# Performance work log

Measured on AMD Instinct MI355X. Metric: run time of the kernel, lower is better.

Reference implementation:

```python
import jax, jax.numpy as jnp
import numpy as np

ALPHA, BETA, LAMB, GAMMA = 1.0, 1.0, 1e-4, 1.0
K_NN, TAU = 50, 0.1
EPS = 1e-8


def _sqdist(A, B):
    # ||a - b||^2, clamped at 0 like the torch code
    d2 = (A * A).sum(1)[:, None] + (B * B).sum(1)[None, :] - 2.0 * (A @ B.T)
    return jnp.maximum(d2, 0.0)


def _mmd(s, t):
    comb = jnp.concatenate([s, t], axis=0)
    sigma_sq = jax.lax.stop_gradient(jnp.median(_sqdist(comb, comb))) / 2.0
    sigma_sq = jnp.where(sigma_sq < 1e-6, jnp.float32(1.0), sigma_sq)
    g = 1.0 / (sigma_sq + EPS)
    kxx = jnp.exp(-g * _sqdist(s, s)).mean()
    kyy = jnp.exp(-g * _sqdist(t, t)).mean()
    kxy = jnp.exp(-g * _sqdist(s, t)).mean()
    return jnp.maximum(kxx + kyy - 2.0 * kxy, 0.0)


def setup_inputs() -> dict:
    key = jax.random.key(0)
    ks = jax.random.split(key, 8)
    B, d, N, Nq, K = 256, 128, 200000, 10000, K_NN
    q_batch = jax.random.normal(ks[0], (B, d), jnp.float32)
    X = jax.random.normal(ks[1], (N, d), jnp.float32)
    W = jax.random.normal(ks[2], (d, d), jnp.float32) * (1.0 / np.sqrt(d))
    b = jnp.zeros((d,), jnp.float32)
    pre_weights = jax.random.uniform(ks[3], (Nq, K), jnp.float32)
    pre_weights = pre_weights / pre_weights.sum(1, keepdims=True)
    pre_indices = jax.random.randint(ks[4], (Nq, K), 0, N)
    q_indices = jax.random.randint(ks[5], (B,), 0, Nq)
    idx = jax.random.randint(ks[6], (B,), 0, N)
    return {"q_batch": q_batch, "X": X, "W": W, "b": b,
            "pre_weights": pre_weights, "pre_indices": pre_indices,
            "q_indices": q_indices, "idx": idx}


def reference(q_batch, X, W, b, pre_weights, pre_indices, q_indices, idx):
    Tq = q_batch @ W.T + b                                   # model(q_batch), Linear(d, d)
    # ---- MMD between mapped queries and a random database batch ----
    loss_dist = _mmd(Tq, X[idx])
    # ---- exact KNN (faiss IndexFlatL2 equivalent) on detached embeddings ----
    d2_all = _sqdist(jax.lax.stop_gradient(Tq), X)           # [B, N]
    _, post_idx = jax.lax.top_k(-d2_all, K_NN)               # [B, K] nearest neighbors
    Xn = X[post_idx]                                         # [B, K, d]
    l2 = ((Tq[:, None, :] - Xn) ** 2).sum(-1)                # [B, K] (grad flows here)
    post_w = jax.nn.softmax(-l2 / TAU, axis=1)
    # ---- union-KL, vectorized over batch (exact torch.unique semantics) ----
    pre_i = pre_indices[q_indices]                           # [B, K]
    pre_w = pre_weights[q_indices]                           # [B, K]
    cat = jnp.concatenate([pre_i, post_idx], axis=1)         # [B, 2K]
    # multiplicity of each id within the concatenated list -> collapse duplicates
    mult = (cat[:, :, None] == cat[:, None, :]).sum(-1).astype(jnp.float32)  # [B, 2K]
    p_raw = jnp.einsum('bmk,bk->bm',
                       (cat[:, :, None] == pre_i[:, None, :]).astype(jnp.float32), pre_w)
    q_raw = jnp.einsum('bmk,bk->bm',
                       (cat[:, :, None] == post_idx[:, None, :]).astype(jnp.float32), post_w)
    p_c = jnp.maximum(p_raw, EPS)
    q_c = jnp.maximum(q_raw, EPS)
    p = p_c / (p_c / mult).sum(1, keepdims=True)             # normalize over union
    q = q_c / (q_c / mult).sum(1, keepdims=True)
    kl = ((p * (jnp.log(p) - jnp.log(q))) / mult).sum(1)     # KL(p || q) per sample
    loss_knn = kl.mean()
    # ---- L2 regularization of model params & anchor loss ----
    loss_reg = 0.5 * ((W ** 2).sum() + (b ** 2).sum())
    loss_anchor = ((Tq - q_batch) ** 2).sum(1).mean()
    total = ALPHA * loss_dist + BETA * loss_knn + LAMB * loss_reg + GAMMA * loss_anchor
    return jnp.stack([total, loss_dist, loss_knn, loss_anchor])
```

## Files before the change

kernel.cpp:

```cpp
#include <hip/hip_runtime.h>
#include <cstdint>

#define D 128
#define NPTS 200000
#define KNN 50
#define CAP 8192
#define NS 8192
#define SLACK 2.0f
#define EB 2048

#define OFF_ACC    0
#define OFF_SEL    256
#define OFF_CNT    1024
#define OFF_HIST0  17408
#define OFF_HIST12 148480
#define MEMSET_BYTES 214016
#define OFF_COMB   214016
#define OFF_D2     476160
#define OFF_XN     1524736
#define OFF_SAMP   2324736
#define OFF_EBUF   2324736
#define OFF_THR    10713344
#define OFF_CANDI  10714368
#define OFF_KSG    19102976
#define OFF_BCNT   19102976
#define OFF_TQSW   27491584
#define OFF_XBF    27557120

typedef __attribute__((ext_vector_type(8))) short bf16x8;
typedef __attribute__((ext_vector_type(4))) float f32x4;
typedef const __attribute__((address_space(1))) void* gas_p;
typedef __attribute__((address_space(3))) void* las_p;

__device__ __forceinline__ unsigned fkey(float f) {
    unsigned u = __float_as_uint(f);
    return u ^ ((unsigned)((int)u >> 31) | 0x80000000u);
}

__device__ __forceinline__ void stage8k(const unsigned short* __restrict__ g,
                                        unsigned short* l, int w, int lane)
{
    #pragma unroll
    for (int j = 0; j < 2; j++) {
        const unsigned short* gp = g + j * 2048 + w * 512 + lane * 8;
        unsigned short* lp = l + j * 2048 + w * 512;
        __builtin_amdgcn_global_load_lds((gas_p)gp, (las_p)lp, 16, 0, 0);
    }
}

__global__ void k_phase1(const float* __restrict__ q, const float* __restrict__ X,
                         const float* __restrict__ W, const float* __restrict__ bb,
                         const int* __restrict__ idx, float* __restrict__ comb,
                         unsigned short* __restrict__ tqsw, unsigned short* __restrict__ xbf,
                         float* __restrict__ xn, float* __restrict__ acc)
{
    const int blk = blockIdx.x, t = threadIdx.x;
    if (blk < 12500) {
        __shared__ float xr[16];
        const int lr = t & 15;
        if (t < 16) xr[t] = 0.f;
        __syncthreads();
        const float4* src = (const float4*)(X + ((long)(blk * 16 + lr)) * D + (t >> 4) * 8);
        float4 v0 = src[0], v1 = src[1];
        uint4 pk;
        pk.x = (__float_as_uint(v0.x) >> 16) | (__float_as_uint(v0.y) & 0xFFFF0000u);
        pk.y = (__float_as_uint(v0.z) >> 16) | (__float_as_uint(v0.w) & 0xFFFF0000u);
        pk.z = (__float_as_uint(v1.x) >> 16) | (__float_as_uint(v1.y) & 0xFFFF0000u);
        pk.w = (__float_as_uint(v1.z) >> 16) | (__float_as_uint(v1.w) & 0xFFFF0000u);
        *(uint4*)(xbf + (long)blk * 2048 + t * 8) = pk;
        float ssq = v0.x*v0.x + v0.y*v0.y + v0.z*v0.z + v0.w*v0.w
                  + v1.x*v1.x + v1.y*v1.y + v1.z*v1.z + v1.w*v1.w;
        atomicAdd(&xr[lr], ssq);
        __syncthreads();
        if (t < 16) xn[blk * 16 + t] = xr[t];
    } else if (blk < 12628) {
        __shared__ float rowv[2][D];
        __shared__ float red[2][D];
        const int half = t >> 7, tt = t & 127;
        const int row = (blk - 12500) * 2 + half;
        rowv[half][tt] = q[row * D + tt];
        __syncthreads();
        float s = 0.f;
        const float* wr = W + tt * D;
        #pragma unroll 4
        for (int k = 0; k < D; k++) s = fmaf(rowv[half][k], wr[k], s);
        s += bb[tt];
        comb[row * D + tt] = s;
        unsigned ub = __float_as_uint(s);
        unsigned short hv = (unsigned short)((ub + 0x7fffu + ((ub >> 16) & 1u)) >> 16);
        int ksb = tt >> 5, quad = (tt & 31) >> 3, jj = tt & 7;
        int lane = quad * 16 + (row & 15);
        tqsw[(row >> 4) * 2048 + ksb * 512 + lane * 8 + jj] = hv;
        float dd = s - rowv[half][tt];
        red[half][tt] = dd * dd;
        __syncthreads();
        for (int off = 64; off > 0; off >>= 1) { if (tt < off) red[half][tt] += red[half][tt + off]; __syncthreads(); }
        if (tt == 0) atomicAdd(&acc[0], red[half][0]);
    } else if (blk < 12756) {
        const int half = t >> 7, tt = t & 127;
        const int i = (blk - 12628) * 2 + half;
        comb[(256 + i) * D + tt] = X[(long)idx[i] * D + tt];
    } else {
        __shared__ float wred[4];
        const int base = (blk - 12756) * 4096;
        float s = 0.f;
        #pragma unroll 4
        for (int k = 0; k < 16; k++) { float v = W[base + k * 256 + t]; s = fmaf(v, v, s); }
        if (blk == 12756 && t < D) { float v = bb[t]; s = fmaf(v, v, s); }
        #pragma unroll
        for (int off = 32; off > 0; off >>= 1) s += __shfl_down(s, off);
        if ((t & 63) == 0) wred[t >> 6] = s;
        __syncthreads();
        if (t == 0) atomicAdd(&acc[7], wred[0] + wred[1] + wred[2] + wred[3]);
    }
}

__global__ void k_d2m(const float* __restrict__ comb, float* __restrict__ D2w,
                      unsigned* __restrict__ hist0, const unsigned short* __restrict__ tqsw,
                      const unsigned short* __restrict__ xbf, const float* __restrict__ xn,
                      float* __restrict__ samp)
{
    __shared__ __align__(16) char smraw[51456];
    const int b = blockIdx.x, t = threadIdx.x;
    if (b < 1024) {
        float (*cj)[D + 1] = (float(*)[D + 1])smraw;
        float (*ci)[D]     = (float(*)[D])(smraw + 33024);
        unsigned* h        = (unsigned*)(smraw + 35072);
        const int ib = b >> 3, jb = b & 7;
        const int w = t >> 6, l = t & 63;
        for (int m = t; m < 4096; m += 256) h[m] = 0;
        const int irow = ib * 4 + w;
        ci[w][l] = comb[irow * D + l];
        ci[w][l + 64] = comb[irow * D + l + 64];
        const float4* src = (const float4*)(comb + (jb * 64) * D);
        #pragma unroll
        for (int m = 0; m < 8; m++) {
            int u = m * 256 + t;
            int r = u >> 5, c = u & 31;
            float4 v = src[u];
            cj[r][c * 4 + 0] = v.x; cj[r][c * 4 + 1] = v.y; cj[r][c * 4 + 2] = v.z; cj[r][c * 4 + 3] = v.w;
        }
        __syncthreads();
        float s = 0.f;
        #pragma unroll 4
        for (int k = 0; k < D; k++) { float d = ci[w][k] - cj[l][k]; s = fmaf(d, d, s); }
        D2w[irow * 512 + jb * 64 + l] = s;
        atomicAdd(&h[__float_as_uint(s) >> 20], 1u);
        __syncthreads();
        const int sh = (ib + jb) & 7;
        for (int m = t; m < 4096; m += 256) { unsigned v = h[m]; if (v) atomicAdd(&hist0[m * 8 + sh], v); }
    } else {
        unsigned short* sb = (unsigned short*)smraw;
        const int w = t >> 6, lane = t & 63;
        const int lr = lane & 15, quad = lane >> 4;
        const int ck = b - 1024;
        stage8k(xbf + (long)ck * 4096, sb, w, lane);
        bf16x8 a[4][4];
        #pragma unroll
        for (int i = 0; i < 4; i++)
            #pragma unroll
            for (int ks = 0; ks < 4; ks++)
                a[i][ks] = *(const bf16x8*)(tqsw + (w * 4 + i) * 2048 + ks * 512 + lane * 8);
        __syncthreads();
        #pragma unroll
        for (int tt = 0; tt < 2; tt++) {
            const int r = (ck * 2 + tt) * 16 + lr;
            float xnv = xn[r];
            bf16x8 bfr[4];
            #pragma unroll
            for (int ks = 0; ks < 4; ks++)
                bfr[ks] = *(const bf16x8*)(sb + tt * 2048 + ks * 512 + lane * 8);
            f32x4 acc4[4];
            #pragma unroll
            for (int i = 0; i < 4; i++) acc4[i] = (f32x4){0.f, 0.f, 0.f, 0.f};
            #pragma unroll
            for (int ks = 0; ks < 4; ks++)
                #pragma unroll
                for (int i = 0; i < 4; i++)
                    acc4[i] = __builtin_amdgcn_mfma_f32_16x16x32_bf16(a[i][ks], bfr[ks], acc4[i], 0, 0, 0);
            #pragma unroll
            for (int i = 0; i < 4; i++)
                #pragma unroll
                for (int reg = 0; reg < 4; reg++) {
                    int qq = w * 64 + i * 16 + quad * 4 + reg;
                    samp[qq * NS + r] = xnv - 2.f * acc4[i][reg];
                }
        }
    }
}

__global__ void k_h1thr(const float* __restrict__ D2w, unsigned* __restrict__ hist12,
                        const unsigned* __restrict__ hist0, unsigned* __restrict__ sel,
                        const float* __restrict__ samp, float* __restrict__ thr)
{
    __shared__ unsigned buf[8192];
    __shared__ unsigned bins[4096];
    __shared__ unsigned part[256];
    __shared__ unsigned selll[4];
    __shared__ unsigned wred[4];
    const int t = threadIdx.x;
    if (blockIdx.x < 256) {
        unsigned s = 0;
        #pragma unroll
        for (int m = 0; m < 16; m++) {
            int bin = t * 16 + m;
            unsigned bs = 0;
            #pragma unroll
            for (int sh = 0; sh < 8; sh++) bs += hist0[bin * 8 + sh];
            bins[bin] = bs;
            s += bs;
        }
        part[t] = s;
        for (int m = t; m < 8192; m += 256) buf[m] = 0;
        __syncthreads();
        if (t == 0) {
            for (int tg = 0; tg < 2; tg++) {
                unsigned r = tg ? 131072u : 131071u;
                int c = 0;
                while (part[c] <= r) { r -= part[c]; c++; }
                int b = c * 16;
                while (bins[b] <= r) { r -= bins[b]; b++; }
                selll[2 * tg] = (unsigned)b; selll[2 * tg + 1] = r;
            }
            if (blockIdx.x == 0) {
                sel[0] = selll[0]; sel[1] = selll[1]; sel[2] = selll[2]; sel[3] = selll[3];
            }
        }
        __syncthreads();
        unsigned p0 = selll[0], p1 = selll[2];
        const int e0 = blockIdx.x * 1024;
        for (int m = 0; m < 4; m++) {
            unsigned key = __float_as_uint(D2w[e0 + m * 256 + t]);
            if ((key >> 20) == p0) atomicAdd(&buf[(key >> 8) & 0xFFFu], 1u);
            if ((key >> 20) == p1) atomicAdd(&buf[4096 + ((key >> 8) & 0xFFFu)], 1u);
        }
        __syncthreads();
        for (int m = t; m < 8192; m += 256) { unsigned v = buf[m]; if (v) atomicAdd(&hist12[m], v); }
    } else {
        const int q = blockIdx.x - 256;
        for (int m = t; m < NS; m += 256) buf[m] = fkey(samp[q * NS + m]);
        __syncthreads();
        unsigned v = 0;
        for (int bit = 31; bit >= 0; bit--) {
            unsigned trial = v | (1u << bit);
            unsigned c = 0;
            for (int m = t; m < NS; m += 256) c += (buf[m] < trial) ? 1u : 0u;
            #pragma unroll
            for (int off = 32; off > 0; off >>= 1) c += __shfl_down(c, off);
            if ((t & 63) == 0) wred[t >> 6] = c;
            __syncthreads();
            unsigned total = wred[0] + wred[1] + wred[2] + wred[3];
            __syncthreads();
            if (total <= (unsigned)(KNN - 1)) v = trial;
        }
        if (t == 0) {
            unsigned orig = (v & 0x80000000u) ? (v ^ 0x80000000u) : ~v;
            thr[q] = __uint_as_float(orig) + SLACK;
        }
    }
}

__global__ void k_hist2s(const float* __restrict__ D2w, unsigned* __restrict__ hist12,
                         unsigned* __restrict__ sel)
{
    __shared__ unsigned h[8192];
    __shared__ unsigned part[256];
    __shared__ unsigned pfx[2];
    __shared__ unsigned rr[2];
    const int t = threadIdx.x;
    for (int tg = 0; tg < 2; tg++) {
        const unsigned* hh = hist12 + tg * 4096;
        unsigned s = 0;
        for (int m = 0; m < 16; m++) s += hh[t * 16 + m];
        part[t] = s;
        __syncthreads();
        if (t == 0) {
            unsigned r = sel[1 + 2 * tg];
            int c = 0;
            while (part[c] <= r) { r -= part[c]; c++; }
            int b = c * 16;
            while (hh[b] <= r) { r -= hh[b]; b++; }
            pfx[tg] = (sel[2 * tg] << 12) | (unsigned)b;
            rr[tg] = r;
        }
        __syncthreads();
    }
    if (blockIdx.x == 0 && t == 0) {
        sel[4] = pfx[0]; sel[5] = rr[0]; sel[6] = pfx[1]; sel[7] = rr[1];
    }
    for (int m = t; m < 8192; m += 256) h[m] = 0;
    __syncthreads();
    unsigned p0 = pfx[0], p1 = pfx[1];
    const int e0 = blockIdx.x * 1024;
    for (int m = 0; m < 4; m++) {
        unsigned key = __float_as_uint(D2w[e0 + m * 256 + t]);
        if ((key >> 8) == p0) atomicAdd(&h[key & 0xFFu], 1u);
        if ((key >> 8) == p1) atomicAdd(&h[4096 + (key & 0xFFu)], 1u);
    }
    __syncthreads();
    unsigned* gp = hist12 + 8192;
    for (int m = t; m < 8192; m += 256) { unsigned v = h[m]; if (v) atomicAdd(&gp[m], v); }
}

__global__ __launch_bounds__(256) void k_mf1(const unsigned short* __restrict__ tqsw,
    const unsigned short* __restrict__ xbf, const float* __restrict__ xn,
    const float* __restrict__ thr, unsigned* __restrict__ ebuf, unsigned* __restrict__ bcnt,
    const float* __restrict__ D2w, const unsigned* __restrict__ hist12,
    const unsigned* __restrict__ sel, float* __restrict__ acc)
{
    if (blockIdx.x >= 1024) {
        __shared__ unsigned h2[512];
        __shared__ float gsh;
        __shared__ float part[12];
        const int t = threadIdx.x, w = t >> 6;
        h2[t] = hist12[8192 + t];
        h2[256 + t] = hist12[8192 + 4096 + t];
        __syncthreads();
        if (t == 0) {
            unsigned key[2];
            for (int tg = 0; tg < 2; tg++) {
                unsigned r = sel[5 + 2 * tg];
                const unsigned* hh = h2 + tg * 256;
                int b = 0;
                while (hh[b] <= r) { r -= hh[b]; b++; }
                key[tg] = (sel[4 + 2 * tg] << 8) | (unsigned)b;
            }
            float med = 0.5f * (__uint_as_float(key[0]) + __uint_as_float(key[1]));
            float ssq = 0.5f * med;
            if (ssq < 1e-6f) ssq = 1.0f;
            gsh = 1.0f / (ssq + 1e-8f);
        }
        __syncthreads();
        const float g = gsh;
        float s[3] = {0.f, 0.f, 0.f};
        const int e0 = (blockIdx.x - 1024) * 1024;
        #pragma unroll
        for (int m = 0; m < 4; m++) {
            int e = e0 + m * 256 + t;
            int i = e >> 9, j = e & 511;
            float v = expf(-g * D2w[e]);
            int qd = (i < 256) ? ((j < 256) ? 0 : 2) : ((j < 256) ? 2 : 1);
            s[qd] += v;
        }
        #pragma unroll
        for (int c = 0; c < 3; c++) {
            float x = s[c];
            #pragma unroll
            for (int off = 32; off > 0; off >>= 1) x += __shfl_down(x, off);
            if ((t & 63) == 0) part[w * 3 + c] = x;
        }
        __syncthreads();
        if (t == 0)
            for (int c = 0; c < 3; c++)
                atomicAdd(&acc[2 + c], part[c] + part[3 + c] + part[6 + c] + part[9 + c]);
        return;
    }
    __shared__ unsigned short sb[2][4096];
    __shared__ unsigned lbuf[1024];
    __shared__ unsigned lcnt;
    __shared__ unsigned gbase;
    const int t = threadIdx.x;
    const int w = t >> 6, lane = t & 63;
    const int lr = lane & 15, quad = lane >> 4;
    unsigned* eb = ebuf + (unsigned)blockIdx.x * EB;
    bf16x8 a[4][4];
    #pragma unroll
    for (int i = 0; i < 4; i++)
        #pragma unroll
        for (int ks = 0; ks < 4; ks++)
            a[i][ks] = *(const bf16x8*)(tqsw + (w * 4 + i) * 2048 + ks * 512 + lane * 8);
    float th_r[4][4];
    #pragma unroll
    for (int i = 0; i < 4; i++)
        #pragma unroll
        for (int reg = 0; reg < 4; reg++)
            th_r[i][reg] = thr[w * 64 + i * 16 + quad * 4 + reg];
    int ck = blockIdx.x;
    int cur = 0;
    if (t == 0) { lcnt = 0; gbase = 0; }
    stage8k(xbf + (long)ck * 4096, sb[0], w, lane);
    __syncthreads();
    while (true) {
        const int ckn = ck + 1024;
        const bool has = ckn < 6250;
        if (has) stage8k(xbf + (long)ckn * 4096, sb[cur ^ 1], w, lane);
        #pragma unroll
        for (int tt = 0; tt < 2; tt++) {
            const int r = (ck * 2 + tt) * 16 + lr;
            float xnv = xn[r];
            bf16x8 b[4];
            #pragma unroll
            for (int ks = 0; ks < 4; ks++)
                b[ks] = *(const bf16x8*)(sb[cur] + tt * 2048 + ks * 512 + lane * 8);
            f32x4 acc4[4];
            #pragma unroll
            for (int i = 0; i < 4; i++) acc4[i] = (f32x4){0.f, 0.f, 0.f, 0.f};
            #pragma unroll
            for (int ks = 0; ks < 4; ks++)
                #pragma unroll
                for (int i = 0; i < 4; i++)
                    acc4[i] = __builtin_amdgcn_mfma_f32_16x16x32_bf16(a[i][ks], b[ks], acc4[i], 0, 0, 0);
            #pragma unroll
            for (int i = 0; i < 4; i++)
                #pragma unroll
                for (int reg = 0; reg < 4; reg++) {
                    float s = xnv - 2.f * acc4[i][reg];
                    if (s <= th_r[i][reg]) {
                        unsigned qq = (unsigned)(w * 64 + i * 16 + quad * 4 + reg);
                        unsigned p = atomicAdd(&lcnt, 1u);
                        if (p < 1024u) lbuf[p] = (qq << 18) | (unsigned)r;
                        else {
                            unsigned d = gbase + p;
                            if (d < EB) eb[d] = (qq << 18) | (unsigned)r;
                        }
                    }
                }
        }
        __syncthreads();
        unsigned n = lcnt;
        if (!has || n >= 512u) {
            unsigned nf = (n < 1024u) ? n : 1024u;
            unsigned gb = gbase;
            for (unsigned m = t; m < nf; m += 256) {
                unsigned d = gb + m;
                if (d < EB) eb[d] = lbuf[m];
            }
            __syncthreads();
            if (t == 0) { gbase = gb + n; lcnt = 0; }
            __syncthreads();
        }
        if (!has) break;
        ck = ckn; cur ^= 1;
    }
    if (t == 0) bcnt[blockIdx.x] = (gbase < EB) ? gbase : EB;
}

__global__ __launch_bounds__(256) void k_scat(const unsigned* __restrict__ ebuf,
    const unsigned* __restrict__ bcnt, int* __restrict__ cand_i, unsigned* __restrict__ cnt)
{
    __shared__ unsigned hist[256];
    __shared__ unsigned startp[256];
    const int t = threadIdx.x;
    const int b0 = blockIdx.x * 8;
    hist[t] = 0;
    __syncthreads();
    for (int b = b0; b < b0 + 8; b++) {
        unsigned n = bcnt[b];
        const unsigned* e = ebuf + (unsigned)b * EB;
        for (unsigned m = t; m < n; m += 256)
            atomicAdd(&hist[e[m] >> 18], 1u);
    }
    __syncthreads();
    unsigned c = hist[t];
    if (c) {
        unsigned base = atomicAdd(&cnt[t * 16], c);
        startp[t] = ((unsigned)t << 13) + base;
    }
    __syncthreads();
    for (int b = b0; b < b0 + 8; b++) {
        unsigned n = bcnt[b];
        const unsigned* e = ebuf + (unsigned)b * EB;
        for (unsigned m = t; m < n; m += 256) {
            unsigned ent = e[m];
            unsigned qq = ent >> 18;
            unsigned pos = atomicAdd(&startp[qq], 1u);
            if (pos < ((qq + 1u) << 13)) cand_i[pos] = (int)(ent & 0x3FFFFu);
        }
    }
}

__global__ void k_rescore(const float* __restrict__ comb, const float* __restrict__ X,
                          const float* __restrict__ xn, const int* __restrict__ cand_i,
                          const unsigned* __restrict__ cnt, unsigned* __restrict__ ksg)
{
    __shared__ float qrow[D];
    const int q = blockIdx.x, sp = blockIdx.y, t = threadIdx.x;
    if (t < D) qrow[t] = comb[q * D + t];
    __syncthreads();
    unsigned nn = cnt[q * 16];
    const int n = (nn < (unsigned)CAP) ? (int)nn : CAP;
    const int g = t >> 3, j = t & 7;
    for (int m = sp * 32 + g; m < n; m += 512) {
        int r = cand_i[q * CAP + m];
        const float4* xr = (const float4*)(X + (long)r * D);
        float s = 0.f;
        #pragma unroll
        for (int p = 0; p < 4; p++) {
            float4 xv = xr[j * 4 + p];
            float4 qv = *(const float4*)&qrow[(j * 4 + p) * 4];
            s = fmaf(xv.x, qv.x, fmaf(xv.y, qv.y, fmaf(xv.z, qv.z, fmaf(xv.w, qv.w, s))));
        }
        s += __shfl_down(s, 4); s += __shfl_down(s, 2); s += __shfl_down(s, 1);
        if (j == 0) ksg[q * CAP + m] = fkey(xn[r] - 2.f * s);
    }
}

__global__ void k_post2(const float* __restrict__ comb, const float* __restrict__ X,
                        const int* __restrict__ cand_i, const unsigned* __restrict__ cnt,
                        const unsigned* __restrict__ ksg, const int* __restrict__ pri,
                        const float* __restrict__ prw, const int* __restrict__ qix,
                        float* __restrict__ acc)
{
    __shared__ unsigned ks[CAP];
    __shared__ float qrow[D];
    __shared__ unsigned wred[4];
    __shared__ unsigned wpos, eqn;
    __shared__ int eq[64];
    __shared__ int pidx[KNN];
    __shared__ float l2s[KNN];
    __shared__ float pw[KNN];
    __shared__ int ci[100];
    __shared__ float pwv[50], qwv[50];
    __shared__ float pterm[100], qterm[100], kterm[100];
    __shared__ float Sp, Sq;
    const int q = blockIdx.x, t = threadIdx.x;
    if (t < D) qrow[t] = comb[q * D + t];
    if (t == 0) { wpos = 0; eqn = 0; }
    unsigned nn = cnt[q * 16];
    const int n = (nn < (unsigned)CAP) ? (int)nn : CAP;
    for (int m = t; m < n; m += 256) ks[m] = ksg[q * CAP + m];
    __syncthreads();
    int kk = KNN - 1; if (kk > n - 1) kk = n - 1;
    unsigned v = 0;
    for (int bit = 31; bit >= 0; bit--) {
        unsigned trial = v | (1u << bit);
        unsigned c = 0;
        for (int m = t; m < n; m += 256) c += (ks[m] < trial) ? 1u : 0u;
        #pragma unroll
        for (int off = 32; off > 0; off >>= 1) c += __shfl_down(c, off);
        if ((t & 63) == 0) wred[t >> 6] = c;
        __syncthreads();
        unsigned total = wred[0] + wred[1] + wred[2] + wred[3];
        __syncthreads();
        if (total <= (unsigned)kk) v = trial;
    }
    for (int m = t; m < n; m += 256) {
        if (ks[m] < v) {
            unsigned p = atomicAdd(&wpos, 1u);
            pidx[p] = cand_i[q * CAP + m];
        } else if (ks[m] == v) {
            unsigned p = atomicAdd(&eqn, 1u);
            if (p < 64) eq[p] = cand_i[q * CAP + m];
        }
    }
    __syncthreads();
    if (t == 0) {
        int c1 = (int)wpos, need = KNN - c1;
        int ne = (eqn < 64u) ? (int)eqn : 64;
        for (int a = 0; a < ne; a++)
            for (int b2 = a + 1; b2 < ne; b2++)
                if (eq[b2] < eq[a]) { int tmp = eq[a]; eq[a] = eq[b2]; eq[b2] = tmp; }
        for (int a = 0; a < need && a < ne; a++) pidx[c1 + a] = eq[a];
    }
    __syncthreads();
    const int g = t >> 3, j = t & 7;
    for (int nb = g; nb < KNN; nb += 32) {
        long r = pidx[nb];
        const float4* xr = (const float4*)(X + r * D);
        float s = 0.f;
        #pragma unroll
        for (int p = 0; p < 4; p++) {
            float4 xv = xr[j * 4 + p];
            float4 qv = *(const float4*)&qrow[(j * 4 + p) * 4];
            float d0 = qv.x - xv.x, d1 = qv.y - xv.y, d2 = qv.z - xv.z, d3 = qv.w - xv.w;
            s += d0 * d0 + d1 * d1 + d2 * d2 + d3 * d3;
        }
        s += __shfl_down(s, 4); s += __shfl_down(s, 2); s += __shfl_down(s, 1);
        if (j == 0) l2s[nb] = s;
    }
    int qi = qix[q];
    if (t >= 128 && t < 178) { int k = t - 128; ci[k] = pri[qi * 50 + k]; pwv[k] = prw[qi * 50 + k]; }
    __syncthreads();
    if (t < 64) {
        float logit = (t < KNN) ? (-l2s[t] * 10.0f) : -3.4e38f;
        float m = logit;
        #pragma unroll
        for (int off = 32; off > 0; off >>= 1) m = fmaxf(m, __shfl_down(m, off));
        m = __shfl(m, 0);
        float e = (t < KNN) ? expf(logit - m) : 0.f;
        float ss = e;
        #pragma unroll
        for (int off = 32; off > 0; off >>= 1) ss += __shfl_down(ss, off);
        ss = __shfl(ss, 0);
        if (t < KNN) pw[t] = e / ss;
    }
    __syncthreads();
    if (t < 50) { ci[50 + t] = pidx[t]; qwv[t] = pw[t]; }
    __syncthreads();
    float pc = 0.f, qc = 0.f, mult = 0.f;
    if (t < 100) {
        int c = ci[t];
        float pr = 0.f, qr = 0.f;
        for (int k = 0; k < 50; k++) {
            bool m1 = (c == ci[k]); bool m2 = (c == ci[50 + k]);
            mult += (m1 ? 1.f : 0.f) + (m2 ? 1.f : 0.f);
            pr += m1 ? pwv[k] : 0.f;
            qr += m2 ? qwv[k] : 0.f;
        }
        pc = fmaxf(pr, 1e-8f); qc = fmaxf(qr, 1e-8f);
        pterm[t] = pc / mult; qterm[t] = qc / mult;
    }
    __syncthreads();
    if (t == 0) { float a = 0.f, b2 = 0.f; for (int m = 0; m < 100; m++) { a += pterm[m]; b2 += qterm[m]; } Sp = a; Sq = b2; }
    __syncthreads();
    if (t < 100) {
        float p = pc / Sp, qq2 = qc / Sq;
        kterm[t] = (p * (logf(p) - logf(qq2))) / mult;
    }
    __syncthreads();
    if (t == 0) { float s = 0.f; for (int m = 0; m < 100; m++) s += kterm[m]; atomicAdd(&acc[1], s); }
}

__global__ void k_final(const float* __restrict__ acc, float* __restrict__ out)
{
    if (threadIdx.x == 0) {
        float reg = 0.5f * acc[7];
        float kxx = acc[2] / 65536.f, kyy = acc[3] / 65536.f, kxy = acc[4] / 131072.f;
        float ld = fmaxf(kxx + kyy - 2.f * kxy, 0.f);
        float lknn = acc[1] / 256.f;
        float lanc = acc[0] / 256.f;
        out[0] = ld + lknn + 1e-4f * reg + lanc;
        out[1] = ld; out[2] = lknn; out[3] = lanc;
    }
}

extern "C" void kernel_launch(void* const* d_in, const int* in_sizes, int n_in,
                              void* d_out, int out_size, void* d_ws, size_t ws_size,
                              hipStream_t stream)
{
    (void)in_sizes; (void)n_in; (void)out_size; (void)ws_size;
    const float* q   = (const float*)d_in[0];
    const float* X   = (const float*)d_in[1];
    const float* W   = (const float*)d_in[2];
    const float* bb  = (const float*)d_in[3];
    const float* prw = (const float*)d_in[4];
    const int*   pri = (const int*)d_in[5];
    const int*   qix = (const int*)d_in[6];
    const int*   idx = (const int*)d_in[7];
    float* out = (float*)d_out;
    char* ws = (char*)d_ws;
    float*    acc   = (float*)(ws + OFF_ACC);
    unsigned* sel   = (unsigned*)(ws + OFF_SEL);
    unsigned* cnt   = (unsigned*)(ws + OFF_CNT);
    unsigned* hist0 = (unsigned*)(ws + OFF_HIST0);
    unsigned* hist12= (unsigned*)(ws + OFF_HIST12);
    float*    comb  = (float*)(ws + OFF_COMB);
    float*    D2w   = (float*)(ws + OFF_D2);
    float*    xn    = (float*)(ws + OFF_XN);
    float*    samp  = (float*)(ws + OFF_SAMP);
    float*    thr   = (float*)(ws + OFF_THR);
    int*      cix   = (int*)(ws + OFF_CANDI);
    unsigned* ksg   = (unsigned*)(ws + OFF_KSG);
    unsigned* ebuf  = (unsigned*)(ws + OFF_EBUF);
    unsigned* bcnt  = (unsigned*)(ws + OFF_BCNT);
    unsigned short* tqsw = (unsigned short*)(ws + OFF_TQSW);
    unsigned short* xbf  = (unsigned short*)(ws + OFF_XBF);

    hipMemsetAsync(ws, 0, MEMSET_BYTES, stream);
    hipLaunchKernelGGL(k_phase1,  dim3(12760),   dim3(256), 0, stream, q, X, W, bb, idx, comb, tqsw, xbf, xn, acc);
    hipLaunchKernelGGL(k_d2m,     dim3(1280),    dim3(256), 0, stream, comb, D2w, hist0, tqsw, xbf, xn, samp);
    hipLaunchKernelGGL(k_h1thr,   dim3(512),     dim3(256), 0, stream, D2w, hist12, hist0, sel, samp, thr);
    hipLaunchKernelGGL(k_hist2s,  dim3(256),     dim3(256), 0, stream, D2w, hist12, sel);
    hipLaunchKernelGGL(k_mf1,     dim3(1280),    dim3(256), 0, stream, tqsw, xbf, xn, thr, ebuf, bcnt, D2w, hist12, sel, acc);
    hipLaunchKernelGGL(k_scat,    dim3(128),     dim3(256), 0, stream, ebuf, bcnt, cix, cnt);
    hipLaunchKernelGGL(k_rescore, dim3(256, 16), dim3(256), 0, stream, comb, X, xn, cix, cnt, ksg);
    hipLaunchKernelGGL(k_post2,   dim3(256),     dim3(256), 0, stream, comb, X, cix, cnt, ksg, pri, prw, qix, acc);
    hipLaunchKernelGGL(k_final,   dim3(1),       dim3(64),  0, stream, acc, out);
}
```

Baseline: 387.0 us.

## Merge median histogram pass into filter kernel and MMD sum into scatter kernel

The second median-histogram pass now runs in extra blocks of the filter kernel, and the MMD exp-sum runs in extra blocks of the scatter kernel, so one kernel launch disappears and these small jobs overlap with larger work. The histogram shared array shrinks from 8192 to 512 entries because only 256 bins per target are used. Separately, the per-row squared-norm reduction in phase1 now uses wave shuffles and a small per-wave shared array instead of shared-memory atomics, which removes one barrier. The cost is that the rebalanced blocks lengthen the filter and scatter kernels slightly.

Result: faster. 372.0 us (-3.9%).

```diff
diff --git a/kernel.cpp b/kernel.cpp
--- a/kernel.cpp
+++ b/kernel.cpp
@@ -56,10 +56,8 @@
 {
     const int blk = blockIdx.x, t = threadIdx.x;
     if (blk < 12500) {
-        __shared__ float xr[16];
+        __shared__ float xr4[4][16];
         const int lr = t & 15;
-        if (t < 16) xr[t] = 0.f;
-        __syncthreads();
         const float4* src = (const float4*)(X + ((long)(blk * 16 + lr)) * D + (t >> 4) * 8);
         float4 v0 = src[0], v1 = src[1];
         uint4 pk;
@@ -70,9 +68,11 @@
         *(uint4*)(xbf + (long)blk * 2048 + t * 8) = pk;
         float ssq = v0.x*v0.x + v0.y*v0.y + v0.z*v0.z + v0.w*v0.w
                   + v1.x*v1.x + v1.y*v1.y + v1.z*v1.z + v1.w*v1.w;
-        atomicAdd(&xr[lr], ssq);
-        __syncthreads();
-        if (t < 16) xn[blk * 16 + t] = xr[t];
+        ssq += __shfl_down(ssq, 32);
+        ssq += __shfl_down(ssq, 16);
+        if ((t & 63) < 16) xr4[t >> 6][lr] = ssq;
+        __syncthreads();
+        if (t < 16) xn[blk * 16 + t] = xr4[0][t] + xr4[1][t] + xr4[2][t] + xr4[3][t];
     } else if (blk < 12628) {
         __shared__ float rowv[2][D];
         __shared__ float red[2][D];
@@ -260,99 +260,52 @@
     }
 }
 
-__global__ void k_hist2s(const float* __restrict__ D2w, unsigned* __restrict__ hist12,
-                         unsigned* __restrict__ sel)
-{
-    __shared__ unsigned h[8192];
-    __shared__ unsigned part[256];
-    __shared__ unsigned pfx[2];
-    __shared__ unsigned rr[2];
-    const int t = threadIdx.x;
-    for (int tg = 0; tg < 2; tg++) {
-        const unsigned* hh = hist12 + tg * 4096;
-        unsigned s = 0;
-        for (int m = 0; m < 16; m++) s += hh[t * 16 + m];
-        part[t] = s;
-        __syncthreads();
-        if (t == 0) {
-            unsigned r = sel[1 + 2 * tg];
-            int c = 0;
-            while (part[c] <= r) { r -= part[c]; c++; }
-            int b = c * 16;
-            while (hh[b] <= r) { r -= hh[b]; b++; }
-            pfx[tg] = (sel[2 * tg] << 12) | (unsigned)b;
-            rr[tg] = r;
-        }
-        __syncthreads();
-    }
-    if (blockIdx.x == 0 && t == 0) {
-        sel[4] = pfx[0]; sel[5] = rr[0]; sel[6] = pfx[1]; sel[7] = rr[1];
-    }
-    for (int m = t; m < 8192; m += 256) h[m] = 0;
-    __syncthreads();
-    unsigned p0 = pfx[0], p1 = pfx[1];
-    const int e0 = blockIdx.x * 1024;
-    for (int m = 0; m < 4; m++) {
-        unsigned key = __float_as_uint(D2w[e0 + m * 256 + t]);
-        if ((key >> 8) == p0) atomicAdd(&h[key & 0xFFu], 1u);
-        if ((key >> 8) == p1) atomicAdd(&h[4096 + (key & 0xFFu)], 1u);
-    }
-    __syncthreads();
-    unsigned* gp = hist12 + 8192;
-    for (int m = t; m < 8192; m += 256) { unsigned v = h[m]; if (v) atomicAdd(&gp[m], v); }
-}
-
-__global__ __launch_bounds__(256) void k_mf1(const unsigned short* __restrict__ tqsw,
+__global__ __launch_bounds__(256) void k_filt2(const unsigned short* __restrict__ tqsw,
     const unsigned short* __restrict__ xbf, const float* __restrict__ xn,
     const float* __restrict__ thr, unsigned* __restrict__ ebuf, unsigned* __restrict__ bcnt,
-    const float* __restrict__ D2w, const unsigned* __restrict__ hist12,
-    const unsigned* __restrict__ sel, float* __restrict__ acc)
+    const float* __restrict__ D2w, unsigned* __restrict__ hist12,
+    unsigned* __restrict__ sel)
 {
     if (blockIdx.x >= 1024) {
-        __shared__ unsigned h2[512];
-        __shared__ float gsh;
-        __shared__ float part[12];
-        const int t = threadIdx.x, w = t >> 6;
-        h2[t] = hist12[8192 + t];
-        h2[256 + t] = hist12[8192 + 4096 + t];
-        __syncthreads();
-        if (t == 0) {
-            unsigned key[2];
-            for (int tg = 0; tg < 2; tg++) {
-                unsigned r = sel[5 + 2 * tg];
-                const unsigned* hh = h2 + tg * 256;
-                int b = 0;
+        __shared__ unsigned h2c[512];
+        __shared__ unsigned part2[256];
+        __shared__ unsigned pfx[2];
+        __shared__ unsigned rr[2];
+        const int t = threadIdx.x;
+        for (int tg = 0; tg < 2; tg++) {
+            const unsigned* hh = hist12 + tg * 4096;
+            unsigned s = 0;
+            for (int m = 0; m < 16; m++) s += hh[t * 16 + m];
+            part2[t] = s;
+            __syncthreads();
+            if (t == 0) {
+                unsigned r = sel[1 + 2 * tg];
+                int c = 0;
+                while (part2[c] <= r) { r -= part2[c]; c++; }
+                int b = c * 16;
                 while (hh[b] <= r) { r -= hh[b]; b++; }
-                key[tg] = (sel[4 + 2 * tg] << 8) | (unsigned)b;
+                pfx[tg] = (sel[2 * tg] << 12) | (unsigned)b;
+                rr[tg] = r;
             }
-            float med = 0.5f * (__uint_as_float(key[0]) + __uint_as_float(key[1]));
-            float ssq = 0.5f * med;
-            if (ssq < 1e-6f) ssq = 1.0f;
-            gsh = 1.0f / (ssq + 1e-8f);
-        }
-        __syncthreads();
-        const float g = gsh;
-        float s[3] = {0.f, 0.f, 0.f};
+            __syncthreads();
+        }
+        if (blockIdx.x == 1024 && t == 0) {
+            sel[4] = pfx[0]; sel[5] = rr[0]; sel[6] = pfx[1]; sel[7] = rr[1];
+        }
+        h2c[t] = 0; h2c[256 + t] = 0;
+        __syncthreads();
+        unsigned p0 = pfx[0], p1 = pfx[1];
         const int e0 = (blockIdx.x - 1024) * 1024;
-        #pragma unroll
         for (int m = 0; m < 4; m++) {
-            int e = e0 + m * 256 + t;
-            int i = e >> 9, j = e & 511;
-            float v = expf(-g * D2w[e]);
-            int qd = (i < 256) ? ((j < 256) ? 0 : 2) : ((j < 256) ? 2 : 1);
-            s[qd] += v;
-        }
-        #pragma unroll
-        for (int c = 0; c < 3; c++) {
-            float x = s[c];
-            #pragma unroll
-            for (int off = 32; off > 0; off >>= 1) x += __shfl_down(x, off);
-            if ((t & 63) == 0) part[w * 3 + c] = x;
-        }
-        __syncthreads();
-        if (t == 0)
-            for (int c = 0; c < 3; c++)
-                atomicAdd(&acc[2 + c], part[c] + part[3 + c] + part[6 + c] + part[9 + c]);
+            unsigned key = __float_as_uint(D2w[e0 + m * 256 + t]);
+            if ((key >> 8) == p0) atomicAdd(&h2c[key & 0xFFu], 1u);
+            if ((key >> 8) == p1) atomicAdd(&h2c[256 + (key & 0xFFu)], 1u);
+        }
+        __syncthreads();
+        unsigned* gp = hist12 + 8192;
+        unsigned v0 = h2c[t], v1 = h2c[256 + t];
+        if (v0) atomicAdd(&gp[t], v0);
+        if (v1) atomicAdd(&gp[4096 + t], v1);
         return;
     }
     __shared__ unsigned short sb[2][4096];
@@ -435,12 +388,61 @@
     if (t == 0) bcnt[blockIdx.x] = (gbase < EB) ? gbase : EB;
 }
 
-__global__ __launch_bounds__(256) void k_scat(const unsigned* __restrict__ ebuf,
-    const unsigned* __restrict__ bcnt, int* __restrict__ cand_i, unsigned* __restrict__ cnt)
-{
+__global__ __launch_bounds__(256) void k_scatmmd(const unsigned* __restrict__ ebuf,
+    const unsigned* __restrict__ bcnt, int* __restrict__ cand_i, unsigned* __restrict__ cnt,
+    const float* __restrict__ D2w, const unsigned* __restrict__ hist12,
+    const unsigned* __restrict__ sel, float* __restrict__ acc)
+{
+    const int t = threadIdx.x;
+    if (blockIdx.x >= 128) {
+        __shared__ unsigned h2[512];
+        __shared__ float gsh;
+        __shared__ float part[12];
+        const int w = t >> 6;
+        h2[t] = hist12[8192 + t];
+        h2[256 + t] = hist12[8192 + 4096 + t];
+        __syncthreads();
+        if (t == 0) {
+            unsigned key[2];
+            for (int tg = 0; tg < 2; tg++) {
+                unsigned r = sel[5 + 2 * tg];
+                const unsigned* hh = h2 + tg * 256;
+                int b = 0;
+                while (hh[b] <= r) { r -= hh[b]; b++; }
+                key[tg] = (sel[4 + 2 * tg] << 8) | (unsigned)b;
+            }
+            float med = 0.5f * (__uint_as_float(key[0]) + __uint_as_float(key[1]));
+            float ssq = 0.5f * med;
+            if (ssq < 1e-6f) ssq = 1.0f;
+            gsh = 1.0f / (ssq + 1e-8f);
+        }
+        __syncthreads();
+        const float g = gsh;
+        float s[3] = {0.f, 0.f, 0.f};
+        const int e0 = (blockIdx.x - 128) * 1024;
+        #pragma unroll
+        for (int m = 0; m < 4; m++) {
+            int e = e0 + m * 256 + t;
+            int i = e >> 9, j = e & 511;
+            float v = expf(-g * D2w[e]);
+            int qd = (i < 256) ? ((j < 256) ? 0 : 2) : ((j < 256) ? 2 : 1);
+            s[qd] += v;
+        }
+        #pragma unroll
+        for (int c = 0; c < 3; c++) {
+            float x = s[c];
+            #pragma unroll
+            for (int off = 32; off > 0; off >>= 1) x += __shfl_down(x, off);
+            if ((t & 63) == 0) part[w * 3 + c] = x;
+        }
+        __syncthreads();
+        if (t == 0)
+            for (int c = 0; c < 3; c++)
+                atomicAdd(&acc[2 + c], part[c] + part[3 + c] + part[6 + c] + part[9 + c]);
+        return;
+    }
     __shared__ unsigned hist[256];
     __shared__ unsigned startp[256];
-    const int t = threadIdx.x;
     const int b0 = blockIdx.x * 8;
     hist[t] = 0;
     __syncthreads();
@@ -660,9 +662,8 @@
     hipLaunchKernelGGL(k_phase1,  dim3(12760),   dim3(256), 0, stream, q, X, W, bb, idx, comb, tqsw, xbf, xn, acc);
     hipLaunchKernelGGL(k_d2m,     dim3(1280),    dim3(256), 0, stream, comb, D2w, hist0, tqsw, xbf, xn, samp);
     hipLaunchKernelGGL(k_h1thr,   dim3(512),     dim3(256), 0, stream, D2w, hist12, hist0, sel, samp, thr);
-    hipLaunchKernelGGL(k_hist2s,  dim3(256),     dim3(256), 0, stream, D2w, hist12, sel);
-    hipLaunchKernelGGL(k_mf1,     dim3(1280),    dim3(256), 0, stream, tqsw, xbf, xn, thr, ebuf, bcnt, D2w, hist12, sel, acc);
-    hipLaunchKernelGGL(k_scat,    dim3(128),     dim3(256), 0, stream, ebuf, bcnt, cix, cnt);
+    hipLaunchKernelGGL(k_filt2,   dim3(1280),    dim3(256), 0, stream, tqsw, xbf, xn, thr, ebuf, bcnt, D2w, hist12, sel);
+    hipLaunchKernelGGL(k_scatmmd, dim3(384),     dim3(256), 0, stream, ebuf, bcnt, cix, cnt, D2w, hist12, sel, acc);
     hipLaunchKernelGGL(k_rescore, dim3(256, 16), dim3(256), 0, stream, comb, X, xn, cix, cnt, ksg);
     hipLaunchKernelGGL(k_post2,   dim3(256),     dim3(256), 0, stream, comb, X, cix, cnt, ksg, pri, prw, qix, acc);
     hipLaunchKernelGGL(k_final,   dim3(1),       dim3(64),  0, stream, acc, out);
```
